# Performance work log

Hardware: AMD Instinct MI355X
Metric: run time of the kernel (lower is better)

Reference implementation:

```python
import jax, jax.numpy as jnp
import numpy as np
from jax import lax

EPS = 1e-5
N_NODES = 128
OUT_SIZE = 128


def conv1d(x_ncw, w_oiw, bias):
    # x: (N, C_in, W), w: (C_out, C_in, K), padding=2 ('same' for K=5)
    y = lax.conv_general_dilated(x_ncw, w_oiw, window_strides=(1,),
                                 padding=[(2, 2)],
                                 dimension_numbers=('NCH', 'OIH', 'NCH'))
    return y + bias[None, :, None]


def bn_ncw(x, g, b):
    # BatchNorm1d over (N, W) per channel, training-mode batch stats (biased var)
    m = jnp.mean(x, axis=(0, 2), keepdims=True)
    v = jnp.var(x, axis=(0, 2), keepdims=True)
    return (x - m) * jax.lax.rsqrt(v + EPS) * g[None, :, None] + b[None, :, None]


def bn_nf(x, g, b):
    # BatchNorm1d over N per feature
    m = jnp.mean(x, axis=0, keepdims=True)
    v = jnp.var(x, axis=0, keepdims=True)
    return (x - m) * jax.lax.rsqrt(v + EPS) * g[None, :] + b[None, :]


def setup_inputs() -> dict:
    key = jax.random.key(0)
    ks = jax.random.split(key, 16)
    B, L = 16, 1024
    inp = {
        'x': jax.random.normal(ks[0], (B, L, 8), dtype=jnp.float32),
        'b': jax.random.uniform(ks[1], (B, L, N_NODES), dtype=jnp.float32),
        'conv1_w': jax.random.normal(ks[2], (32, 8, 5), dtype=jnp.float32) * (1.0 / np.sqrt(8 * 5)),
        'conv1_b': jnp.zeros((32,), dtype=jnp.float32),
        'bn1_g': jnp.ones((32,), dtype=jnp.float32),
        'bn1_b': jnp.zeros((32,), dtype=jnp.float32),
        'conv2_w': jax.random.normal(ks[3], (64, 32, 5), dtype=jnp.float32) * (1.0 / np.sqrt(32 * 5)),
        'conv2_b': jnp.zeros((64,), dtype=jnp.float32),
        'bn2_g': jnp.ones((64,), dtype=jnp.float32),
        'bn2_b': jnp.zeros((64,), dtype=jnp.float32),
        'w1': jax.random.normal(ks[4], (100, N_NODES * 64), dtype=jnp.float32) * (1.0 / np.sqrt(N_NODES * 64)),
        'b1': jnp.zeros((100,), dtype=jnp.float32),
        'bn3_g': jnp.ones((100,), dtype=jnp.float32),
        'bn3_b': jnp.zeros((100,), dtype=jnp.float32),
        'w2': jax.random.normal(ks[5], (OUT_SIZE, 100), dtype=jnp.float32) * (1.0 / np.sqrt(100)),
        'b2': jnp.zeros((OUT_SIZE,), dtype=jnp.float32),
    }
    return inp


def reference(x, b, conv1_w, conv1_b, bn1_g, bn1_b, conv2_w, conv2_b,
              bn2_g, bn2_b, w1, b1, bn3_g, bn3_b, w2, b2):
    n = x.shape[0]
    # temporal: Conv1d->BN->ReLU x2, operating on (N, C, L)
    h = jnp.swapaxes(x, 1, 2)                       # (N, 8, L)
    h = jax.nn.relu(bn_ncw(conv1d(h, conv1_w, conv1_b), bn1_g, bn1_b))
    h = jax.nn.relu(bn_ncw(conv1d(h, conv2_w, conv2_b), bn2_g, bn2_b))
    h = jnp.swapaxes(h, 1, 2)                       # (N, L, 64)
    # pooling: z[n,j,k] = max_i b[n,i,j] * h[n,i,k]
    y = b[:, :, :, None] * h[:, :, None, :]          # (N, L, n_nodes, 64)
    z = jnp.max(y, axis=1)                          # (N, n_nodes, 64)
    z = z.reshape(n, -1)                            # (N, n_nodes*64)
    # spatial: Linear->BN->ReLU->Linear
    z = jax.nn.relu(bn_nf(z @ w1.T + b1, bn3_g, bn3_b))
    return z @ w2.T + b2
```

## Files before the change

### kernel.cpp

```cpp
#include <hip/hip_runtime.h>

#define EPS 1e-5f

#define BATCH 16
#define LEN   1024
#define C0    8
#define C1    32
#define C2    64
#define NODES 128
#define NF1   100
#define NF2   128

#define OFF_C1   0
#define OFF_C2   524288
#define OFF_S1P  1572864
#define OFF_S2P  1589248
#define OFF_ZZP  1622016
#define OFF_CNT  1647616

__global__ __launch_bounds__(256)
void kA(const float* __restrict__ x, const float* __restrict__ w,
        const float* __restrict__ bias, float* __restrict__ c1,
        float* __restrict__ s1p) {
    int tid = threadIdx.x, b = blockIdx.x;
    int lane = tid & 63, wave = tid >> 6;
    int n = b >> 4, lt = b & 15;
    int l = lt * 64 + lane;
    int cg8 = __builtin_amdgcn_readfirstlane(wave * 8);

    float xr[5][8];
#pragma unroll
    for (int dl = 0; dl < 5; ++dl) {
        int lw = l + dl - 2;
        if (lw >= 0 && lw < LEN) {
            const float4* p = (const float4*)(x + ((size_t)n * LEN + lw) * C0);
            float4 a = p[0], b4 = p[1];
            xr[dl][0] = a.x;  xr[dl][1] = a.y;  xr[dl][2] = a.z;  xr[dl][3] = a.w;
            xr[dl][4] = b4.x; xr[dl][5] = b4.y; xr[dl][6] = b4.z; xr[dl][7] = b4.w;
        } else {
#pragma unroll
            for (int ci = 0; ci < 8; ++ci) xr[dl][ci] = 0.f;
        }
    }
#pragma unroll
    for (int u = 0; u < 8; ++u) {
        int c = cg8 + u;
        float acc = bias[c];
        const float* wc = w + c * 40;
#pragma unroll
        for (int ci = 0; ci < 8; ++ci)
#pragma unroll
            for (int dl = 0; dl < 5; ++dl)
                acc += xr[dl][ci] * wc[ci * 5 + dl];
        c1[((size_t)n * C1 + c) * LEN + l] = acc;

        float s = acc, q = acc * acc;
#pragma unroll
        for (int off = 32; off >= 1; off >>= 1) {
            s += __shfl_xor(s, off);
            q += __shfl_xor(q, off);
        }
        if (lane == 0) {
            s1p[b * 64 + c * 2]     = s;
            s1p[b * 64 + c * 2 + 1] = q;
        }
    }
}

__global__ __launch_bounds__(256)
void kB(const float* __restrict__ c1, const float* __restrict__ w,
        const float* __restrict__ bias,
        const float* __restrict__ g1, const float* __restrict__ bb1,
        const float* __restrict__ s1p,
        float* __restrict__ c2, float* __restrict__ s2p,
        unsigned* __restrict__ cnt) {
    int tid = threadIdx.x, b = blockIdx.x;
    int lane = tid & 63, wave = tid >> 6;

    if (b == 0 && tid == 0) cnt[0] = 0u;

    __shared__ float sc1[32], sh1[32];
    __shared__ __align__(16) float a1[32 * 68];
    __shared__ float redw[256];

    {
        float a0=0,a1_=0,a2=0,a3=0,a4=0,a5=0,a6=0,a7=0;
        int b0 = wave * 64;
        for (int i = 0; i < 64; i += 8) {
            a0  += s1p[(size_t)(b0+i  ) * 64 + lane];
            a1_ += s1p[(size_t)(b0+i+1) * 64 + lane];
            a2  += s1p[(size_t)(b0+i+2) * 64 + lane];
            a3  += s1p[(size_t)(b0+i+3) * 64 + lane];
            a4  += s1p[(size_t)(b0+i+4) * 64 + lane];
            a5  += s1p[(size_t)(b0+i+5) * 64 + lane];
            a6  += s1p[(size_t)(b0+i+6) * 64 + lane];
            a7  += s1p[(size_t)(b0+i+7) * 64 + lane];
        }
        redw[wave * 64 + lane] = ((a0+a1_)+(a2+a3)) + ((a4+a5)+(a6+a7));
    }
    __syncthreads();
    if (tid < 64)
        redw[tid] = redw[tid] + redw[64 + tid] + redw[128 + tid] + redw[192 + tid];
    __syncthreads();
    if (tid < 32) {
        float s = redw[tid * 2], q = redw[tid * 2 + 1];
        float mean = s * (1.f / 16384.f);
        float var  = q * (1.f / 16384.f) - mean * mean;
        float rs   = rsqrtf(var + EPS);
        float sc   = g1[tid] * rs;
        sc1[tid] = sc;
        sh1[tid] = bb1[tid] - mean * sc;
    }
    __syncthreads();

    int n = b >> 4, lt = b & 15;
    int lbase = lt * 64;

    for (int idx = tid; idx < 32 * 68; idx += 256) {
        int ci = idx / 68, lo = idx - ci * 68;
        int lg = lbase + lo - 2;
        float v = 0.f;
        if (lg >= 0 && lg < LEN) v = c1[((size_t)n * C1 + ci) * LEN + lg];
        a1[idx] = fmaxf(0.f, v * sc1[ci] + sh1[ci]);
    }
    __syncthreads();

    int l = lane;
    int cobase = __builtin_amdgcn_readfirstlane(wave * 16);

    float acc[16];
#pragma unroll
    for (int u = 0; u < 16; ++u) acc[u] = bias[cobase + u];

    for (int ci = 0; ci < 32; ++ci) {
        float v0 = a1[ci * 68 + l + 0];
        float v1 = a1[ci * 68 + l + 1];
        float v2 = a1[ci * 68 + l + 2];
        float v3 = a1[ci * 68 + l + 3];
        float v4 = a1[ci * 68 + l + 4];
#pragma unroll
        for (int u = 0; u < 16; ++u) {
            const float* wp = w + ((size_t)(cobase + u) * 32 + ci) * 5;
            acc[u] += v0 * wp[0] + v1 * wp[1] + v2 * wp[2] + v3 * wp[3] + v4 * wp[4];
        }
    }

    int lg = lbase + l;
#pragma unroll
    for (int u = 0; u < 16; ++u)
        c2[((size_t)n * C2 + cobase + u) * LEN + lg] = acc[u];

    for (int u = 0; u < 16; ++u) {
        float s = acc[u], q = acc[u] * acc[u];
#pragma unroll
        for (int off = 32; off >= 1; off >>= 1) {
            s += __shfl_xor(s, off);
            q += __shfl_xor(q, off);
        }
        if (lane == 0) {
            int c = cobase + u;
            s2p[b * 128 + c * 2]     = s;
            s2p[b * 128 + c * 2 + 1] = q;
        }
    }
}

__global__ __launch_bounds__(256)
void kC(const float* __restrict__ bmat, const float* __restrict__ c2,
        const float* __restrict__ g2, const float* __restrict__ bb2,
        const float* __restrict__ s2p, const float* __restrict__ w1,
        const float* __restrict__ b1f, const float* __restrict__ g3,
        const float* __restrict__ b3, const float* __restrict__ w2,
        const float* __restrict__ b2f,
        float* __restrict__ zzp, unsigned* __restrict__ cnt,
        float* __restrict__ out) {
    int tid = threadIdx.x, b = blockIdx.x;
    int lane = tid & 63, wave = tid >> 6;
    int n = b >> 4, jt = (b >> 2) & 3, ks = b & 3;
    int jbase = jt * 32, kbase = ks * 16;

    __shared__ __align__(16) float smem[4224];
    __shared__ unsigned sflag;
    float* red2 = smem;
    float* sc2s = smem + 256;
    float* sh2s = smem + 320;
    float* bt   = smem + 384;
    float* ht   = smem + 2496;
    float* zsl  = smem + 3648;

    {
        int v = tid & 127, half = tid >> 7;
        float a0=0,a1=0,a2=0,a3=0,a4=0,a5=0,a6=0,a7=0;
        int b0 = half * 128;
        for (int i = 0; i < 128; i += 8) {
            a0 += s2p[(size_t)(b0+i  ) * 128 + v];
            a1 += s2p[(size_t)(b0+i+1) * 128 + v];
            a2 += s2p[(size_t)(b0+i+2) * 128 + v];
            a3 += s2p[(size_t)(b0+i+3) * 128 + v];
            a4 += s2p[(size_t)(b0+i+4) * 128 + v];
            a5 += s2p[(size_t)(b0+i+5) * 128 + v];
            a6 += s2p[(size_t)(b0+i+6) * 128 + v];
            a7 += s2p[(size_t)(b0+i+7) * 128 + v];
        }
        red2[half * 128 + v] = ((a0+a1)+(a2+a3)) + ((a4+a5)+(a6+a7));
    }
    __syncthreads();
    if (tid < 128) red2[tid] += red2[128 + tid];
    __syncthreads();
    if (tid < 64) {
        float s = red2[tid * 2], q = red2[tid * 2 + 1];
        float mean = s * (1.f / 16384.f);
        float var  = q * (1.f / 16384.f) - mean * mean;
        float rs   = rsqrtf(var + EPS);
        float sc   = g2[tid] * rs;
        sc2s[tid] = sc;
        sh2s[tid] = bb2[tid] - mean * sc;
    }
    __syncthreads();

    int jl = tid >> 3, kl2 = (tid & 7) * 2;
    float mx0 = 0.f, mx1 = 0.f;

    int il = tid >> 2, jq = tid & 3;
    int cc = tid >> 4, iq = tid & 15;
    float scl = sc2s[kbase + cc], shl = sh2s[kbase + cc];

    float4 pb0, pb1, pc0, pc1 = {};
    {
        const float4* p = (const float4*)(bmat + ((size_t)n * LEN + il) * NODES + jbase + jq * 8);
        pb0 = p[0]; pb1 = p[1];
        pc0 = *(const float4*)(c2 + ((size_t)n * C2 + kbase + cc) * LEN + iq * 4);
    }

    for (int it = 0; it < 16; ++it) {
        __syncthreads();
        {
            float* d = &bt[il * 33 + jq * 8];
            d[0] = pb0.x; d[1] = pb0.y; d[2] = pb0.z; d[3] = pb0.w;
            d[4] = pb1.x; d[5] = pb1.y; d[6] = pb1.z; d[7] = pb1.w;
            int i0 = iq * 4;
            ht[(i0 + 0) * 18 + cc] = fmaxf(0.f, pc0.x * scl + shl);
            ht[(i0 + 1) * 18 + cc] = fmaxf(0.f, pc0.y * scl + shl);
            ht[(i0 + 2) * 18 + cc] = fmaxf(0.f, pc0.z * scl + shl);
            ht[(i0 + 3) * 18 + cc] = fmaxf(0.f, pc0.w * scl + shl);
        }
        __syncthreads();
        if (it + 1 < 16) {
            int ib = (it + 1) * 64;
            const float4* p = (const float4*)(bmat + ((size_t)n * LEN + ib + il) * NODES + jbase + jq * 8);
            pb0 = p[0]; pb1 = p[1];
            pc0 = *(const float4*)(c2 + ((size_t)n * C2 + kbase + cc) * LEN + ib + iq * 4);
        }
#pragma unroll 8
        for (int i = 0; i < 64; ++i) {
            float bv = bt[i * 33 + jl];
            float2 hv = *(const float2*)&ht[i * 18 + kl2];
            mx0 = fmaxf(mx0, bv * hv.x);
            mx1 = fmaxf(mx1, bv * hv.y);
        }
    }
    __syncthreads();
    zsl[jl * 16 + kl2]     = mx0;
    zsl[jl * 16 + kl2 + 1] = mx1;
    __syncthreads();

    {
        int slice = jt * 4 + ks;
        float4 z0 = *(const float4*)&zsl[lane * 8];
        float4 z1 = *(const float4*)&zsl[lane * 8 + 4];
        const float* wb = w1 + (size_t)(wave * 25) * 8192
                        + (size_t)(jbase + (lane >> 1)) * 64 + kbase + (lane & 1) * 8;
        float s[25];
#pragma unroll
        for (int t = 0; t < 25; ++t) {
            const float* wp = wb + (size_t)t * 8192;
            float4 w0 = *(const float4*)wp;
            float4 w1v = *(const float4*)(wp + 4);
            s[t] = z0.x*w0.x + z0.y*w0.y + z0.z*w0.z + z0.w*w0.w
                 + z1.x*w1v.x + z1.y*w1v.y + z1.z*w1v.z + z1.w*w1v.w;
        }
#pragma unroll
        for (int t = 0; t < 25; ++t) {
            float v = s[t];
#pragma unroll
            for (int off = 32; off >= 1; off >>= 1) v += __shfl_xor(v, off);
            if (lane == 0)
                atomicExch(&zzp[(size_t)slice * 1600 + n * 100 + wave * 25 + t], v);
        }
    }

    asm volatile("s_waitcnt vmcnt(0)" ::: "memory");
    __syncthreads();
    if (tid == 0) {
        unsigned prev = atomicAdd(cnt, 1u);
        sflag = (prev == 255u) ? 1u : 0u;
    }
    __syncthreads();
    if (!sflag) return;

    float* zzl = smem;
    float* sc3 = smem + 1600;
    float* sh3 = smem + 1700;

    for (int i4 = tid; i4 < 400; i4 += 256) {
        float4 a = make_float4(0.f, 0.f, 0.f, 0.f);
#pragma unroll
        for (int sI = 0; sI < 16; ++sI) {
            float4 v = *(const float4*)&zzp[(size_t)sI * 1600 + i4 * 4];
            a.x += v.x; a.y += v.y; a.z += v.z; a.w += v.w;
        }
        int flat = i4 * 4;
        zzl[flat + 0] = a.x + b1f[(flat + 0) % 100];
        zzl[flat + 1] = a.y + b1f[(flat + 1) % 100];
        zzl[flat + 2] = a.z + b1f[(flat + 2) % 100];
        zzl[flat + 3] = a.w + b1f[(flat + 3) % 100];
    }
    __syncthreads();
    if (tid < NF1) {
        float s = 0.f, q = 0.f;
#pragma unroll
        for (int m = 0; m < BATCH; ++m) {
            float v = zzl[m * NF1 + tid];
            s += v; q += v * v;
        }
        float mean = s * (1.f / 16.f);
        float var  = q * (1.f / 16.f) - mean * mean;
        float rs   = rsqrtf(var + EPS);
        float sc   = g3[tid] * rs;
        sc3[tid] = sc;
        sh3[tid] = b3[tid] - mean * sc;
    }
    __syncthreads();
    for (int t = tid; t < BATCH * NF1; t += 256) {
        int f = t % NF1;
        zzl[t] = fmaxf(0.f, zzl[t] * sc3[f] + sh3[f]);
    }
    __syncthreads();
    {
        int o = tid & 127, half = tid >> 7;
        float acc[8];
#pragma unroll
        for (int nn = 0; nn < 8; ++nn) acc[nn] = b2f[o];
        const float* wr = w2 + (size_t)o * NF1;
        for (int f = 0; f < NF1; ++f) {
            float wvv = wr[f];
#pragma unroll
            for (int nn = 0; nn < 8; ++nn)
                acc[nn] += zzl[(half * 8 + nn) * NF1 + f] * wvv;
        }
#pragma unroll
        for (int nn = 0; nn < 8; ++nn)
            out[(half * 8 + nn) * NF2 + o] = acc[nn];
    }
}

extern "C" void kernel_launch(void* const* d_in, const int* in_sizes, int n_in,
                              void* d_out, int out_size, void* d_ws, size_t ws_size,
                              hipStream_t stream) {
    const float* x    = (const float*)d_in[0];
    const float* bmat = (const float*)d_in[1];
    const float* c1w  = (const float*)d_in[2];
    const float* c1b  = (const float*)d_in[3];
    const float* g1   = (const float*)d_in[4];
    const float* bb1  = (const float*)d_in[5];
    const float* c2w  = (const float*)d_in[6];
    const float* c2b  = (const float*)d_in[7];
    const float* g2   = (const float*)d_in[8];
    const float* bb2  = (const float*)d_in[9];
    const float* w1   = (const float*)d_in[10];
    const float* b1   = (const float*)d_in[11];
    const float* g3   = (const float*)d_in[12];
    const float* b3   = (const float*)d_in[13];
    const float* w2   = (const float*)d_in[14];
    const float* b2   = (const float*)d_in[15];
    float* out = (float*)d_out;
    float* ws  = (float*)d_ws;

    float*    c1  = ws + OFF_C1;
    float*    c2  = ws + OFF_C2;
    float*    s1p = ws + OFF_S1P;
    float*    s2p = ws + OFF_S2P;
    float*    zzp = ws + OFF_ZZP;
    unsigned* cnt = (unsigned*)(ws + OFF_CNT);

    kA<<<256, 256, 0, stream>>>(x, c1w, c1b, c1, s1p);
    kB<<<256, 256, 0, stream>>>(c1, c2w, c2b, g1, bb1, s1p, c2, s2p, cnt);
    kC<<<256, 256, 0, stream>>>(bmat, c2, g2, bb2, s2p, w1, b1, g3, b3, w2, b2,
                                zzp, cnt, out);
}
```

Baseline: 163.0 us.

## Recompute conv1 in kB, atomic BN stats, and larger pooling tiles

```diff
diff --git a/kernel.cpp b/kernel.cpp
--- a/kernel.cpp
+++ b/kernel.cpp
@@ -11,22 +11,29 @@
 #define NF1   100
 #define NF2   128
 
-#define OFF_C1   0
-#define OFF_C2   524288
-#define OFF_S1P  1572864
-#define OFF_S2P  1589248
-#define OFF_ZZP  1622016
-#define OFF_CNT  1647616
+#define OFF_S1T  0
+#define OFF_C2   16384
+#define OFF_ST2  1064960
+#define OFF_ZZ   1065088
+#define OFF_CNT  1066688
+
+#define AL(p) __hip_atomic_load((p), __ATOMIC_RELAXED, __HIP_MEMORY_SCOPE_AGENT)
 
 __global__ __launch_bounds__(256)
 void kA(const float* __restrict__ x, const float* __restrict__ w,
-        const float* __restrict__ bias, float* __restrict__ c1,
-        float* __restrict__ s1p) {
+        const float* __restrict__ bias, float* __restrict__ s1t,
+        float* __restrict__ stats2, float* __restrict__ zz,
+        unsigned* __restrict__ cnt) {
     int tid = threadIdx.x, b = blockIdx.x;
     int lane = tid & 63, wave = tid >> 6;
     int n = b >> 4, lt = b & 15;
     int l = lt * 64 + lane;
-    int cg8 = __builtin_amdgcn_readfirstlane(wave * 8);
+
+    if (b == 0) {
+        if (tid < 128) stats2[tid] = 0.f;
+        for (int t = tid; t < 1600; t += 256) zz[t] = 0.f;
+        if (tid == 0) cnt[0] = 0u;
+    }
 
     float xr[5][8];
 #pragma unroll
@@ -42,6 +49,7 @@
             for (int ci = 0; ci < 8; ++ci) xr[dl][ci] = 0.f;
         }
     }
+    int cg8 = __builtin_amdgcn_readfirstlane(wave * 8);
 #pragma unroll
     for (int u = 0; u < 8; ++u) {
         int c = cg8 + u;
@@ -52,7 +60,6 @@
 #pragma unroll
             for (int dl = 0; dl < 5; ++dl)
                 acc += xr[dl][ci] * wc[ci * 5 + dl];
-        c1[((size_t)n * C1 + c) * LEN + l] = acc;
 
         float s = acc, q = acc * acc;
 #pragma unroll
@@ -61,49 +68,74 @@
             q += __shfl_xor(q, off);
         }
         if (lane == 0) {
-            s1p[b * 64 + c * 2]     = s;
-            s1p[b * 64 + c * 2 + 1] = q;
+            s1t[(c * 2 + 0) * 256 + b] = s;
+            s1t[(c * 2 + 1) * 256 + b] = q;
         }
     }
 }
 
 __global__ __launch_bounds__(256)
-void kB(const float* __restrict__ c1, const float* __restrict__ w,
-        const float* __restrict__ bias,
+void kB(const float* __restrict__ x, const float* __restrict__ c1w,
+        const float* __restrict__ c1b, const float* __restrict__ c2w,
+        const float* __restrict__ c2b,
         const float* __restrict__ g1, const float* __restrict__ bb1,
-        const float* __restrict__ s1p,
-        float* __restrict__ c2, float* __restrict__ s2p,
-        unsigned* __restrict__ cnt) {
+        const float* __restrict__ s1t,
+        float* __restrict__ c2, float* __restrict__ stats2) {
     int tid = threadIdx.x, b = blockIdx.x;
     int lane = tid & 63, wave = tid >> 6;
-
-    if (b == 0 && tid == 0) cnt[0] = 0u;
-
-    __shared__ float sc1[32], sh1[32];
+    int n = b >> 4, lt = b & 15;
+    int lbase = lt * 64;
+
+    __shared__ __align__(16) float xs[72 * 9];
     __shared__ __align__(16) float a1[32 * 68];
     __shared__ float redw[256];
+    __shared__ float fin[64];
+    __shared__ float sc1[32], sh1[32];
+
+    if (tid < 144) {
+        int row = tid >> 1, half = tid & 1;
+        int lg = lbase - 4 + row;
+        float4 v = make_float4(0.f, 0.f, 0.f, 0.f);
+        if (lg >= 0 && lg < LEN)
+            v = *(const float4*)(x + ((size_t)n * LEN + lg) * C0 + half * 4);
+        float* d = &xs[row * 9 + half * 4];
+        d[0] = v.x; d[1] = v.y; d[2] = v.z; d[3] = v.w;
+    }
 
     {
-        float a0=0,a1_=0,a2=0,a3=0,a4=0,a5=0,a6=0,a7=0;
-        int b0 = wave * 64;
-        for (int i = 0; i < 64; i += 8) {
-            a0  += s1p[(size_t)(b0+i  ) * 64 + lane];
-            a1_ += s1p[(size_t)(b0+i+1) * 64 + lane];
-            a2  += s1p[(size_t)(b0+i+2) * 64 + lane];
-            a3  += s1p[(size_t)(b0+i+3) * 64 + lane];
-            a4  += s1p[(size_t)(b0+i+4) * 64 + lane];
-            a5  += s1p[(size_t)(b0+i+5) * 64 + lane];
-            a6  += s1p[(size_t)(b0+i+6) * 64 + lane];
-            a7  += s1p[(size_t)(b0+i+7) * 64 + lane];
-        }
-        redw[wave * 64 + lane] = ((a0+a1_)+(a2+a3)) + ((a4+a5)+(a6+a7));
+        int v = tid >> 2, seg = tid & 3;
+        const float4* p = (const float4*)(s1t + (size_t)v * 256 + seg * 64);
+        float4 a0 = p[0], a1_ = p[1], a2 = p[2], a3 = p[3];
+        float s0 = 0, s1_ = 0, s2 = 0, s3 = 0;
+#pragma unroll
+        for (int i = 0; i < 4; ++i) {
+            float4 b0 = p[i * 4 + 0], b1 = p[i * 4 + 1], b2 = p[i * 4 + 2], b3 = p[i * 4 + 3];
+            s0 += b0.x + b0.y + b0.z + b0.w;
+            s1_ += b1.x + b1.y + b1.z + b1.w;
+            s2 += b2.x + b2.y + b2.z + b2.w;
+            s3 += b3.x + b3.y + b3.z + b3.w;
+        }
+        (void)a0; (void)a1_; (void)a2; (void)a3;
+        redw[tid] = (s0 + s1_) + (s2 + s3);
     }
     __syncthreads();
     if (tid < 64)
-        redw[tid] = redw[tid] + redw[64 + tid] + redw[128 + tid] + redw[192 + tid];
+        fin[tid] = redw[tid * 4] + redw[tid * 4 + 1] + redw[tid * 4 + 2] + redw[tid * 4 + 3];
+
+    for (int idx = tid; idx < 32 * 68; idx += 256) {
+        int ch = idx / 68, lo = idx - ch * 68;
+        float acc = c1b[ch];
+        const float* wc = c1w + ch * 40;
+#pragma unroll
+        for (int ci = 0; ci < 8; ++ci)
+#pragma unroll
+            for (int dl = 0; dl < 5; ++dl)
+                acc += xs[(lo + dl) * 9 + ci] * wc[ci * 5 + dl];
+        a1[idx] = acc;
+    }
     __syncthreads();
     if (tid < 32) {
-        float s = redw[tid * 2], q = redw[tid * 2 + 1];
+        float s = fin[tid * 2], q = fin[tid * 2 + 1];
         float mean = s * (1.f / 16384.f);
         float var  = q * (1.f / 16384.f) - mean * mean;
         float rs   = rsqrtf(var + EPS);
@@ -112,16 +144,11 @@
         sh1[tid] = bb1[tid] - mean * sc;
     }
     __syncthreads();
-
-    int n = b >> 4, lt = b & 15;
-    int lbase = lt * 64;
-
     for (int idx = tid; idx < 32 * 68; idx += 256) {
         int ci = idx / 68, lo = idx - ci * 68;
         int lg = lbase + lo - 2;
-        float v = 0.f;
-        if (lg >= 0 && lg < LEN) v = c1[((size_t)n * C1 + ci) * LEN + lg];
-        a1[idx] = fmaxf(0.f, v * sc1[ci] + sh1[ci]);
+        float v = a1[idx];
+        a1[idx] = (lg >= 0 && lg < LEN) ? fmaxf(0.f, v * sc1[ci] + sh1[ci]) : 0.f;
     }
     __syncthreads();
 
@@ -130,7 +157,7 @@
 
     float acc[16];
 #pragma unroll
-    for (int u = 0; u < 16; ++u) acc[u] = bias[cobase + u];
+    for (int u = 0; u < 16; ++u) acc[u] = c2b[cobase + u];
 
     for (int ci = 0; ci < 32; ++ci) {
         float v0 = a1[ci * 68 + l + 0];
@@ -140,7 +167,7 @@
         float v4 = a1[ci * 68 + l + 4];
 #pragma unroll
         for (int u = 0; u < 16; ++u) {
-            const float* wp = w + ((size_t)(cobase + u) * 32 + ci) * 5;
+            const float* wp = c2w + ((size_t)(cobase + u) * 32 + ci) * 5;
             acc[u] += v0 * wp[0] + v1 * wp[1] + v2 * wp[2] + v3 * wp[3] + v4 * wp[4];
         }
     }
@@ -159,8 +186,8 @@
         }
         if (lane == 0) {
             int c = cobase + u;
-            s2p[b * 128 + c * 2]     = s;
-            s2p[b * 128 + c * 2 + 1] = q;
+            atomicAdd(&stats2[c], s);
+            atomicAdd(&stats2[64 + c], q);
         }
     }
 }
@@ -168,124 +195,113 @@
 __global__ __launch_bounds__(256)
 void kC(const float* __restrict__ bmat, const float* __restrict__ c2,
         const float* __restrict__ g2, const float* __restrict__ bb2,
-        const float* __restrict__ s2p, const float* __restrict__ w1,
+        const float* __restrict__ stats2, const float* __restrict__ w1,
         const float* __restrict__ b1f, const float* __restrict__ g3,
         const float* __restrict__ b3, const float* __restrict__ w2,
         const float* __restrict__ b2f,
-        float* __restrict__ zzp, unsigned* __restrict__ cnt,
+        float* __restrict__ zz, unsigned* __restrict__ cnt,
         float* __restrict__ out) {
     int tid = threadIdx.x, b = blockIdx.x;
     int lane = tid & 63, wave = tid >> 6;
     int n = b >> 4, jt = (b >> 2) & 3, ks = b & 3;
     int jbase = jt * 32, kbase = ks * 16;
 
-    __shared__ __align__(16) float smem[4224];
+    __shared__ __align__(16) float smem[13088];
     __shared__ unsigned sflag;
-    float* red2 = smem;
-    float* sc2s = smem + 256;
-    float* sh2s = smem + 320;
-    float* bt   = smem + 384;
-    float* ht   = smem + 2496;
-    float* zsl  = smem + 3648;
-
-    {
-        int v = tid & 127, half = tid >> 7;
-        float a0=0,a1=0,a2=0,a3=0,a4=0,a5=0,a6=0,a7=0;
-        int b0 = half * 128;
-        for (int i = 0; i < 128; i += 8) {
-            a0 += s2p[(size_t)(b0+i  ) * 128 + v];
-            a1 += s2p[(size_t)(b0+i+1) * 128 + v];
-            a2 += s2p[(size_t)(b0+i+2) * 128 + v];
-            a3 += s2p[(size_t)(b0+i+3) * 128 + v];
-            a4 += s2p[(size_t)(b0+i+4) * 128 + v];
-            a5 += s2p[(size_t)(b0+i+5) * 128 + v];
-            a6 += s2p[(size_t)(b0+i+6) * 128 + v];
-            a7 += s2p[(size_t)(b0+i+7) * 128 + v];
-        }
-        red2[half * 128 + v] = ((a0+a1)+(a2+a3)) + ((a4+a5)+(a6+a7));
-    }
-    __syncthreads();
-    if (tid < 128) red2[tid] += red2[128 + tid];
-    __syncthreads();
-    if (tid < 64) {
-        float s = red2[tid * 2], q = red2[tid * 2 + 1];
+    float* bt   = smem;
+    float* ht   = smem + 8448;
+    float* sc2s = smem + 13056;
+    float* sh2s = smem + 13072;
+
+    if (tid < 16) {
+        int c = kbase + tid;
+        float s = stats2[c], q = stats2[64 + c];
         float mean = s * (1.f / 16384.f);
         float var  = q * (1.f / 16384.f) - mean * mean;
         float rs   = rsqrtf(var + EPS);
-        float sc   = g2[tid] * rs;
+        float sc   = g2[c] * rs;
         sc2s[tid] = sc;
-        sh2s[tid] = bb2[tid] - mean * sc;
-    }
-    __syncthreads();
-
+        sh2s[tid] = bb2[c] - mean * sc;
+    }
+    __syncthreads();
+
+    int il = tid;
+    int cc = tid & 15, ig = tid >> 4;
+    float scl = sc2s[cc], shl = sh2s[cc];
     int jl = tid >> 3, kl2 = (tid & 7) * 2;
     float mx0 = 0.f, mx1 = 0.f;
 
-    int il = tid >> 2, jq = tid & 3;
-    int cc = tid >> 4, iq = tid & 15;
-    float scl = sc2s[kbase + cc], shl = sh2s[kbase + cc];
-
-    float4 pb0, pb1, pc0, pc1 = {};
+    float4 pb[8], pc[4];
     {
-        const float4* p = (const float4*)(bmat + ((size_t)n * LEN + il) * NODES + jbase + jq * 8);
-        pb0 = p[0]; pb1 = p[1];
-        pc0 = *(const float4*)(c2 + ((size_t)n * C2 + kbase + cc) * LEN + iq * 4);
-    }
-
-    for (int it = 0; it < 16; ++it) {
+        const float4* bp = (const float4*)(bmat + ((size_t)n * LEN + il) * NODES + jbase);
+#pragma unroll
+        for (int e = 0; e < 8; ++e) pb[e] = bp[e];
+        const float4* cp = (const float4*)(c2 + ((size_t)n * C2 + kbase + cc) * LEN + ig * 16);
+#pragma unroll
+        for (int r = 0; r < 4; ++r) pc[r] = cp[r];
+    }
+
+    for (int it = 0; it < 4; ++it) {
+        {
+#pragma unroll
+            for (int e = 0; e < 8; ++e)
+                *(float4*)&bt[il * 33 + e * 4] = pb[e];
+#pragma unroll
+            for (int r = 0; r < 4; ++r) {
+                float4 v = pc[r];
+                int i0 = ig * 16 + r * 4;
+                ht[(i0 + 0) * 18 + cc] = fmaxf(0.f, v.x * scl + shl);
+                ht[(i0 + 1) * 18 + cc] = fmaxf(0.f, v.y * scl + shl);
+                ht[(i0 + 2) * 18 + cc] = fmaxf(0.f, v.z * scl + shl);
+                ht[(i0 + 3) * 18 + cc] = fmaxf(0.f, v.w * scl + shl);
+            }
+        }
         __syncthreads();
-        {
-            float* d = &bt[il * 33 + jq * 8];
-            d[0] = pb0.x; d[1] = pb0.y; d[2] = pb0.z; d[3] = pb0.w;
-            d[4] = pb1.x; d[5] = pb1.y; d[6] = pb1.z; d[7] = pb1.w;
-            int i0 = iq * 4;
-            ht[(i0 + 0) * 18 + cc] = fmaxf(0.f, pc0.x * scl + shl);
-            ht[(i0 + 1) * 18 + cc] = fmaxf(0.f, pc0.y * scl + shl);
-            ht[(i0 + 2) * 18 + cc] = fmaxf(0.f, pc0.z * scl + shl);
-            ht[(i0 + 3) * 18 + cc] = fmaxf(0.f, pc0.w * scl + shl);
-        }
-        __syncthreads();
-        if (it + 1 < 16) {
-            int ib = (it + 1) * 64;
-            const float4* p = (const float4*)(bmat + ((size_t)n * LEN + ib + il) * NODES + jbase + jq * 8);
-            pb0 = p[0]; pb1 = p[1];
-            pc0 = *(const float4*)(c2 + ((size_t)n * C2 + kbase + cc) * LEN + ib + iq * 4);
+        if (it < 3) {
+            int ib = (it + 1) * 256;
+            const float4* bp = (const float4*)(bmat + ((size_t)n * LEN + ib + il) * NODES + jbase);
+#pragma unroll
+            for (int e = 0; e < 8; ++e) pb[e] = bp[e];
+            const float4* cp = (const float4*)(c2 + ((size_t)n * C2 + kbase + cc) * LEN + ib + ig * 16);
+#pragma unroll
+            for (int r = 0; r < 4; ++r) pc[r] = cp[r];
         }
 #pragma unroll 8
-        for (int i = 0; i < 64; ++i) {
+        for (int i = 0; i < 256; ++i) {
             float bv = bt[i * 33 + jl];
             float2 hv = *(const float2*)&ht[i * 18 + kl2];
             mx0 = fmaxf(mx0, bv * hv.x);
             mx1 = fmaxf(mx1, bv * hv.y);
         }
-    }
-    __syncthreads();
+        __syncthreads();
+    }
+
+    float* zsl = smem;
     zsl[jl * 16 + kl2]     = mx0;
     zsl[jl * 16 + kl2 + 1] = mx1;
     __syncthreads();
 
     {
-        int slice = jt * 4 + ks;
-        float4 z0 = *(const float4*)&zsl[lane * 8];
-        float4 z1 = *(const float4*)&zsl[lane * 8 + 4];
+        int jloc = lane >> 2, kq = (lane & 3) * 4;
+        float4 za = *(const float4*)&zsl[jloc * 16 + kq];
+        float4 zb = *(const float4*)&zsl[(16 + jloc) * 16 + kq];
         const float* wb = w1 + (size_t)(wave * 25) * 8192
-                        + (size_t)(jbase + (lane >> 1)) * 64 + kbase + (lane & 1) * 8;
+                        + (size_t)(jbase + jloc) * 64 + kbase + kq;
         float s[25];
 #pragma unroll
         for (int t = 0; t < 25; ++t) {
             const float* wp = wb + (size_t)t * 8192;
             float4 w0 = *(const float4*)wp;
-            float4 w1v = *(const float4*)(wp + 4);
-            s[t] = z0.x*w0.x + z0.y*w0.y + z0.z*w0.z + z0.w*w0.w
-                 + z1.x*w1v.x + z1.y*w1v.y + z1.z*w1v.z + z1.w*w1v.w;
+            float4 w1v = *(const float4*)(wp + 16 * 64);
+            s[t] = za.x * w0.x + za.y * w0.y + za.z * w0.z + za.w * w0.w
+                 + zb.x * w1v.x + zb.y * w1v.y + zb.z * w1v.z + zb.w * w1v.w;
         }
 #pragma unroll
         for (int t = 0; t < 25; ++t) {
             float v = s[t];
 #pragma unroll
             for (int off = 32; off >= 1; off >>= 1) v += __shfl_xor(v, off);
-            if (lane == 0)
-                atomicExch(&zzp[(size_t)slice * 1600 + n * 100 + wave * 25 + t], v);
+            if (lane == 0) atomicAdd(&zz[n * NF1 + wave * 25 + t], v);
         }
     }
 
@@ -302,19 +318,8 @@
     float* sc3 = smem + 1600;
     float* sh3 = smem + 1700;
 
-    for (int i4 = tid; i4 < 400; i4 += 256) {
-        float4 a = make_float4(0.f, 0.f, 0.f, 0.f);
-#pragma unroll
-        for (int sI = 0; sI < 16; ++sI) {
-            float4 v = *(const float4*)&zzp[(size_t)sI * 1600 + i4 * 4];
-            a.x += v.x; a.y += v.y; a.z += v.z; a.w += v.w;
-        }
-        int flat = i4 * 4;
-        zzl[flat + 0] = a.x + b1f[(flat + 0) % 100];
-        zzl[flat + 1] = a.y + b1f[(flat + 1) % 100];
-        zzl[flat + 2] = a.z + b1f[(flat + 2) % 100];
-        zzl[flat + 3] = a.w + b1f[(flat + 3) % 100];
-    }
+    for (int t = tid; t < BATCH * NF1; t += 256)
+        zzl[t] = AL(&zz[t]) + b1f[t % NF1];
     __syncthreads();
     if (tid < NF1) {
         float s = 0.f, q = 0.f;
@@ -376,15 +381,14 @@
     float* out = (float*)d_out;
     float* ws  = (float*)d_ws;
 
-    float*    c1  = ws + OFF_C1;
-    float*    c2  = ws + OFF_C2;
-    float*    s1p = ws + OFF_S1P;
-    float*    s2p = ws + OFF_S2P;
-    float*    zzp = ws + OFF_ZZP;
-    unsigned* cnt = (unsigned*)(ws + OFF_CNT);
-
-    kA<<<256, 256, 0, stream>>>(x, c1w, c1b, c1, s1p);
-    kB<<<256, 256, 0, stream>>>(c1, c2w, c2b, g1, bb1, s1p, c2, s2p, cnt);
-    kC<<<256, 256, 0, stream>>>(bmat, c2, g2, bb2, s2p, w1, b1, g3, b3, w2, b2,
-                                zzp, cnt, out);
+    float*    s1t    = ws + OFF_S1T;
+    float*    c2buf  = ws + OFF_C2;
+    float*    stats2 = ws + OFF_ST2;
+    float*    zz     = ws + OFF_ZZ;
+    unsigned* cnt    = (unsigned*)(ws + OFF_CNT);
+
+    kA<<<256, 256, 0, stream>>>(x, c1w, c1b, s1t, stats2, zz, cnt);
+    kB<<<256, 256, 0, stream>>>(x, c1w, c1b, c2w, c2b, g1, bb1, s1t, c2buf, stats2);
+    kC<<<256, 256, 0, stream>>>(bmat, c2buf, g2, bb2, stats2, w1, b1, g3, b3, w2, b2,
+                                zz, cnt, out);
 }
```

New measurement: 268.5 us. 64.7% more time.

## Retile max-pool stage with larger L chunks and per-thread 2x4 register blocking

Applied to the files above, without the earlier changes.

```diff
diff --git a/kernel.cpp b/kernel.cpp
--- a/kernel.cpp
+++ b/kernel.cpp
@@ -17,6 +17,8 @@
 #define OFF_S2P  1589248
 #define OFF_ZZP  1622016
 #define OFF_CNT  1647616
+
+#define AL(p) __hip_atomic_load((p), __ATOMIC_RELAXED, __HIP_MEMORY_SCOPE_AGENT)
 
 __global__ __launch_bounds__(256)
 void kA(const float* __restrict__ x, const float* __restrict__ w,
@@ -179,14 +181,13 @@
     int n = b >> 4, jt = (b >> 2) & 3, ks = b & 3;
     int jbase = jt * 32, kbase = ks * 16;
 
-    __shared__ __align__(16) float smem[4224];
+    __shared__ __align__(16) float smem[14464];
     __shared__ unsigned sflag;
+    float* bt   = smem;
+    float* ht   = smem + 9216;
+    float* sc2s = smem + 14336;
+    float* sh2s = smem + 14352;
     float* red2 = smem;
-    float* sc2s = smem + 256;
-    float* sh2s = smem + 320;
-    float* bt   = smem + 384;
-    float* ht   = smem + 2496;
-    float* zsl  = smem + 3648;
 
     {
         int v = tid & 127, half = tid >> 7;
@@ -207,77 +208,115 @@
     __syncthreads();
     if (tid < 128) red2[tid] += red2[128 + tid];
     __syncthreads();
-    if (tid < 64) {
-        float s = red2[tid * 2], q = red2[tid * 2 + 1];
+    if (tid < 16) {
+        int c = kbase + tid;
+        float s = red2[c * 2], q = red2[c * 2 + 1];
         float mean = s * (1.f / 16384.f);
         float var  = q * (1.f / 16384.f) - mean * mean;
         float rs   = rsqrtf(var + EPS);
-        float sc   = g2[tid] * rs;
+        float sc   = g2[c] * rs;
         sc2s[tid] = sc;
-        sh2s[tid] = bb2[tid] - mean * sc;
-    }
-    __syncthreads();
-
-    int jl = tid >> 3, kl2 = (tid & 7) * 2;
-    float mx0 = 0.f, mx1 = 0.f;
-
-    int il = tid >> 2, jq = tid & 3;
-    int cc = tid >> 4, iq = tid & 15;
-    float scl = sc2s[kbase + cc], shl = sh2s[kbase + cc];
-
-    float4 pb0, pb1, pc0, pc1 = {};
-    {
-        const float4* p = (const float4*)(bmat + ((size_t)n * LEN + il) * NODES + jbase + jq * 8);
-        pb0 = p[0]; pb1 = p[1];
-        pc0 = *(const float4*)(c2 + ((size_t)n * C2 + kbase + cc) * LEN + iq * 4);
-    }
-
-    for (int it = 0; it < 16; ++it) {
+        sh2s[tid] = bb2[c] - mean * sc;
+    }
+    __syncthreads();
+
+    int il = tid;
+    int cc = tid & 15, ig16 = tid >> 4;
+    float scl = sc2s[cc], shl = sh2s[cc];
+
+    int jl = lane >> 2, kg = lane & 3;
+    int irow0 = wave * 64;
+    float mx[2][4];
+#pragma unroll
+    for (int a = 0; a < 2; ++a)
+#pragma unroll
+        for (int c = 0; c < 4; ++c) mx[a][c] = 0.f;
+
+    float4 pb[8], pc[4];
+    {
+        const float4* bp = (const float4*)(bmat + ((size_t)n * LEN + il) * NODES + jbase);
+#pragma unroll
+        for (int e = 0; e < 8; ++e) pb[e] = bp[e];
+        const float4* cp = (const float4*)(c2 + ((size_t)n * C2 + kbase + cc) * LEN + ig16 * 16);
+#pragma unroll
+        for (int r = 0; r < 4; ++r) pc[r] = cp[r];
+    }
+
+    for (int it = 0; it < 4; ++it) {
+        {
+#pragma unroll
+            for (int e = 0; e < 8; ++e)
+                *(float4*)&bt[il * 36 + e * 4] = pb[e];
+#pragma unroll
+            for (int r = 0; r < 4; ++r) {
+                float4 v = pc[r];
+                int i0 = ig16 * 16 + r * 4;
+                ht[(i0 + 0) * 20 + cc] = fmaxf(0.f, v.x * scl + shl);
+                ht[(i0 + 1) * 20 + cc] = fmaxf(0.f, v.y * scl + shl);
+                ht[(i0 + 2) * 20 + cc] = fmaxf(0.f, v.z * scl + shl);
+                ht[(i0 + 3) * 20 + cc] = fmaxf(0.f, v.w * scl + shl);
+            }
+        }
         __syncthreads();
-        {
-            float* d = &bt[il * 33 + jq * 8];
-            d[0] = pb0.x; d[1] = pb0.y; d[2] = pb0.z; d[3] = pb0.w;
-            d[4] = pb1.x; d[5] = pb1.y; d[6] = pb1.z; d[7] = pb1.w;
-            int i0 = iq * 4;
-            ht[(i0 + 0) * 18 + cc] = fmaxf(0.f, pc0.x * scl + shl);
-            ht[(i0 + 1) * 18 + cc] = fmaxf(0.f, pc0.y * scl + shl);
-            ht[(i0 + 2) * 18 + cc] = fmaxf(0.f, pc0.z * scl + shl);
-            ht[(i0 + 3) * 18 + cc] = fmaxf(0.f, pc0.w * scl + shl);
+        if (it < 3) {
+            int ib = (it + 1) * 256;
+            const float4* bp = (const float4*)(bmat + ((size_t)n * LEN + ib + il) * NODES + jbase);
+#pragma unroll
+            for (int e = 0; e < 8; ++e) pb[e] = bp[e];
+            const float4* cp = (const float4*)(c2 + ((size_t)n * C2 + kbase + cc) * LEN + ib + ig16 * 16);
+#pragma unroll
+            for (int r = 0; r < 4; ++r) pc[r] = cp[r];
+        }
+#pragma unroll 4
+        for (int ii = 0; ii < 64; ++ii) {
+            int i = irow0 + ii;
+            float2 bv = *(const float2*)&bt[i * 36 + jl * 2];
+            float4 hv = *(const float4*)&ht[i * 20 + kg * 4];
+            mx[0][0] = fmaxf(mx[0][0], bv.x * hv.x);
+            mx[0][1] = fmaxf(mx[0][1], bv.x * hv.y);
+            mx[0][2] = fmaxf(mx[0][2], bv.x * hv.z);
+            mx[0][3] = fmaxf(mx[0][3], bv.x * hv.w);
+            mx[1][0] = fmaxf(mx[1][0], bv.y * hv.x);
+            mx[1][1] = fmaxf(mx[1][1], bv.y * hv.y);
+            mx[1][2] = fmaxf(mx[1][2], bv.y * hv.z);
+            mx[1][3] = fmaxf(mx[1][3], bv.y * hv.w);
         }
         __syncthreads();
-        if (it + 1 < 16) {
-            int ib = (it + 1) * 64;
-            const float4* p = (const float4*)(bmat + ((size_t)n * LEN + ib + il) * NODES + jbase + jq * 8);
-            pb0 = p[0]; pb1 = p[1];
-            pc0 = *(const float4*)(c2 + ((size_t)n * C2 + kbase + cc) * LEN + ib + iq * 4);
-        }
-#pragma unroll 8
-        for (int i = 0; i < 64; ++i) {
-            float bv = bt[i * 33 + jl];
-            float2 hv = *(const float2*)&ht[i * 18 + kl2];
-            mx0 = fmaxf(mx0, bv * hv.x);
-            mx1 = fmaxf(mx1, bv * hv.y);
-        }
-    }
-    __syncthreads();
-    zsl[jl * 16 + kl2]     = mx0;
-    zsl[jl * 16 + kl2 + 1] = mx1;
+    }
+
+    float* zpart = smem;
+    float* zsl   = smem + 2048;
+#pragma unroll
+    for (int a = 0; a < 2; ++a)
+        *(float4*)&zpart[wave * 512 + (jl * 2 + a) * 16 + kg * 4]
+            = make_float4(mx[a][0], mx[a][1], mx[a][2], mx[a][3]);
+    __syncthreads();
+    {
+        int o = tid * 2;
+        float2 v0 = *(const float2*)&zpart[o];
+        float2 v1 = *(const float2*)&zpart[512 + o];
+        float2 v2 = *(const float2*)&zpart[1024 + o];
+        float2 v3 = *(const float2*)&zpart[1536 + o];
+        zsl[o]     = fmaxf(fmaxf(v0.x, v1.x), fmaxf(v2.x, v3.x));
+        zsl[o + 1] = fmaxf(fmaxf(v0.y, v1.y), fmaxf(v2.y, v3.y));
+    }
     __syncthreads();
 
     {
         int slice = jt * 4 + ks;
-        float4 z0 = *(const float4*)&zsl[lane * 8];
-        float4 z1 = *(const float4*)&zsl[lane * 8 + 4];
+        int jloc = lane >> 2, kq = (lane & 3) * 4;
+        float4 za = *(const float4*)&zsl[jloc * 16 + kq];
+        float4 zb = *(const float4*)&zsl[(16 + jloc) * 16 + kq];
         const float* wb = w1 + (size_t)(wave * 25) * 8192
-                        + (size_t)(jbase + (lane >> 1)) * 64 + kbase + (lane & 1) * 8;
+                        + (size_t)(jbase + jloc) * 64 + kbase + kq;
         float s[25];
 #pragma unroll
         for (int t = 0; t < 25; ++t) {
             const float* wp = wb + (size_t)t * 8192;
             float4 w0 = *(const float4*)wp;
-            float4 w1v = *(const float4*)(wp + 4);
-            s[t] = z0.x*w0.x + z0.y*w0.y + z0.z*w0.z + z0.w*w0.w
-                 + z1.x*w1v.x + z1.y*w1v.y + z1.z*w1v.z + z1.w*w1v.w;
+            float4 w1v = *(const float4*)(wp + 16 * 64);
+            s[t] = za.x * w0.x + za.y * w0.y + za.z * w0.z + za.w * w0.w
+                 + zb.x * w1v.x + zb.y * w1v.y + zb.z * w1v.z + zb.w * w1v.w;
         }
 #pragma unroll
         for (int t = 0; t < 25; ++t) {
@@ -306,7 +345,10 @@
         float4 a = make_float4(0.f, 0.f, 0.f, 0.f);
 #pragma unroll
         for (int sI = 0; sI < 16; ++sI) {
-            float4 v = *(const float4*)&zzp[(size_t)sI * 1600 + i4 * 4];
+            float4 v = make_float4(AL(&zzp[(size_t)sI * 1600 + i4 * 4 + 0]),
+                                   AL(&zzp[(size_t)sI * 1600 + i4 * 4 + 1]),
+                                   AL(&zzp[(size_t)sI * 1600 + i4 * 4 + 2]),
+                                   AL(&zzp[(size_t)sI * 1600 + i4 * 4 + 3]));
             a.x += v.x; a.y += v.y; a.z += v.z; a.w += v.w;
         }
         int flat = i4 * 4;
```

Result: slower. 174.2 us (+6.9%).
